# Optimization experiments

Hardware: AMD Instinct MI355X
Metric: run time of the kernel (lower is better)

Reference implementation:

```python
import jax, jax.numpy as jnp
import numpy as np

# dims
B, L, DIN = 32, 1024, 8
D, KK, S = 128, 16, 8
K = (L - KK) // S + 1  # 127 patch tokens
NB, F = 4, 24
Q = 256.0  # Q8.8 scale


def _ste(x, y):
    # straight-through: forward = y (quantized), backward = identity
    return x + jax.lax.stop_gradient(y - x)


def q88(x):
    q = jnp.clip(jnp.round(x * Q), -32768.0, 32767.0) / Q
    return _ste(x, q)


def sig_lut(x):
    xq = q88(x)
    return q88(jax.nn.sigmoid(xq))


def silu_lut(x):
    xq = q88(x)
    return q88(xq * jax.nn.sigmoid(xq))


def layernorm(x, g, b, eps=1e-5):
    m = jnp.mean(x, axis=-1, keepdims=True)
    v = jnp.mean((x - m) ** 2, axis=-1, keepdims=True)
    return (x - m) * jax.lax.rsqrt(v + eps) * g + b


def conv1x1_q88(x, w, b):
    # x: (B, Cin, L); w: (Cout, Cin); Q8.8 integer-emulated pointwise conv
    y = jnp.einsum('bcl,oc->bol', q88(x), q88(w)) + q88(b)[None, :, None]
    return q88(y)


def conv1d_q88(x, w, b, stride):
    # x: (B, Cin, L); w: (Cout, Cin, k)
    y = jax.lax.conv_general_dilated(q88(x), q88(w), (stride,), 'VALID',
                                     dimension_numbers=('NCH', 'OIH', 'NCH'))
    return q88(y + q88(b)[None, :, None])


def ssm_scan(x, w_dt, b_dt):
    # x: (B, K, D). dt_proj acts along the time axis (Linear K->K), per source.
    # lam_all[b,t,d] = sigmoid_LUT(sum_k x[b,k,d] * w_dt[t,k] + b_dt[t])
    lam = sig_lut(jnp.einsum('bkd,tk->btd', x, w_dt) + b_dt[None, :, None])
    xs = jnp.moveaxis(x, 1, 0)      # (K, B, D)
    lams = jnp.moveaxis(lam, 1, 0)  # (K, B, D)

    def step(s, tu):
        lam_t, u_t = tu
        s = lam_t * s + (1.0 - lam_t) * u_t
        return s, s

    s0 = jnp.zeros(x.shape[::2], dtype=x.dtype)  # (B, D)
    _, ys = jax.lax.scan(step, s0, (lams, xs))
    return jnp.moveaxis(ys, 0, 1)  # (B, K, D)


def setup_inputs() -> dict:
    key = jax.random.key(0)
    ks = jax.random.split(key, 20)
    n = lambda k, sh, s=0.05: (jax.random.normal(k, sh, dtype=jnp.float32) * s)
    return {
        'x': jax.random.normal(ks[0], (B, L, DIN), dtype=jnp.float32),
        'w_proj': n(ks[1], (D, DIN), 0.2), 'b_proj': n(ks[2], (D,), 0.02),
        'w_patch': n(ks[3], (D, D, KK), 0.05), 'b_patch': n(ks[4], (D,), 0.02),
        'pe': n(ks[5], (K, D), 0.5), 'pe_scale': jnp.float32(1.0),
        'ln_g': jnp.ones((NB, D), jnp.float32), 'ln_b': jnp.zeros((NB, D), jnp.float32),
        'w_in': n(ks[6], (NB, D, D), 0.08), 'w_gate': n(ks[7], (NB, D, D), 0.08),
        'w_out': n(ks[8], (NB, D, D), 0.08),
        'w_dt': n(ks[9], (NB, K, K), 0.08), 'b_dt': n(ks[10], (NB, K), 0.02),
        'lnf_g': jnp.ones((D,), jnp.float32), 'lnf_b': jnp.zeros((D,), jnp.float32),
        'w_flat': n(ks[11], (D * F, D, K), 0.02), 'b_flat': n(ks[12], (D * F,), 0.02),
        'w_head': n(ks[13], (2, D), 0.1), 'b_head': n(ks[14], (2,), 0.02),
    }


def reference(x, w_proj, b_proj, w_patch, b_patch, pe, pe_scale,
              ln_g, ln_b, w_in, w_gate, w_out, w_dt, b_dt,
              lnf_g, lnf_b, w_flat, b_flat, w_head, b_head):
    xc = jnp.transpose(x, (0, 2, 1))                # (B, DIN, L)
    xp = conv1x1_q88(xc, w_proj, b_proj)            # (B, D, L)
    xe = conv1d_q88(xp, w_patch, b_patch, S)        # (B, D, K)
    h = jnp.transpose(xe, (0, 2, 1)) + pe_scale * pe[None]  # (B, K, D)
    for i in range(NB):
        hn = layernorm(h, ln_g[i], ln_b[i])
        u = silu_lut(jnp.einsum('bkd,de->bke', hn, w_in[i]))
        y = ssm_scan(u, w_dt[i], b_dt[i])
        g = silu_lut(jnp.einsum('bkd,de->bke', hn, w_gate[i]))
        h = h + jnp.einsum('bkd,de->bke', y * g, w_out[i])
    h = layernorm(h, lnf_g, lnf_b)
    xp2 = jnp.transpose(h, (0, 2, 1))               # (B, D, K)
    # output_layer_flat: full-length Conv1d kernel==K -> one giant contraction
    y_feat = q88(jnp.einsum('bdk,odk->bo', q88(xp2), q88(w_flat)) + q88(b_flat))
    y_feat = y_feat.reshape(x.shape[0], D, F)       # (B, D, F)
    out = conv1x1_q88(y_feat, w_head, b_head)       # (B, 2, F)
    return out
```

## Files before the change

kernel.cpp:

```cpp
#include <hip/hip_runtime.h>
#include <cmath>

#define DEV __device__ __forceinline__

namespace {

constexpr int Kp    = 127;
constexpr int Mrows = 32 * Kp;
constexpr int Rred  = 128 * Kp;

DEV float q88(float x) {
  float r = rintf(x * 256.0f);
  r = fminf(fmaxf(r, -32768.0f), 32767.0f);
  return r * 0.00390625f;
}
DEV float sigmoid_(float x) { return 1.0f / (1.0f + expf(-x)); }

DEV void fma16(const float4 av, const float4 bv, float (&acc)[4][4]) {
  acc[0][0] = fmaf(av.x, bv.x, acc[0][0]); acc[0][1] = fmaf(av.x, bv.y, acc[0][1]);
  acc[0][2] = fmaf(av.x, bv.z, acc[0][2]); acc[0][3] = fmaf(av.x, bv.w, acc[0][3]);
  acc[1][0] = fmaf(av.y, bv.x, acc[1][0]); acc[1][1] = fmaf(av.y, bv.y, acc[1][1]);
  acc[1][2] = fmaf(av.y, bv.z, acc[1][2]); acc[1][3] = fmaf(av.y, bv.w, acc[1][3]);
  acc[2][0] = fmaf(av.z, bv.x, acc[2][0]); acc[2][1] = fmaf(av.z, bv.y, acc[2][1]);
  acc[2][2] = fmaf(av.z, bv.z, acc[2][2]); acc[2][3] = fmaf(av.z, bv.w, acc[2][3]);
  acc[3][0] = fmaf(av.w, bv.x, acc[3][0]); acc[3][1] = fmaf(av.w, bv.y, acc[3][1]);
  acc[3][2] = fmaf(av.w, bv.z, acc[3][2]); acc[3][3] = fmaf(av.w, bv.w, acc[3][3]);
}

__global__ __launch_bounds__(256) void k_quant(
    const float* __restrict__ wproj, const float* __restrict__ bproj,
    const float* __restrict__ wpatch, const float* __restrict__ bpatch,
    const float* __restrict__ whead, const float* __restrict__ bhead,
    const float* __restrict__ bflat,
    float* __restrict__ wq_proj, float* __restrict__ bq_proj, float* __restrict__ wpq,
    float* __restrict__ bq_patch, float* __restrict__ wq_head, float* __restrict__ bq_head,
    float* __restrict__ bq_flat) {
  int i = blockIdx.x * 256 + threadIdx.x;
  if (i < 262144) {
    int j = i >> 14;
    int c = (i >> 7) & 127;
    int d = i & 127;
    wpq[i] = q88(wpatch[(d * 128 + c) * 16 + j]);
  }
  int t = i - 262144;
  if (t >= 0) {
    if      (t < 1024) wq_proj[t]         = q88(wproj[t]);
    else if (t < 1152) bq_proj[t - 1024]  = q88(bproj[t - 1024]);
    else if (t < 1280) bq_patch[t - 1152] = q88(bpatch[t - 1152]);
    else if (t < 1536) wq_head[t - 1280]  = q88(whead[t - 1280]);
    else if (t < 1538) bq_head[t - 1536]  = q88(bhead[t - 1536]);
    else if (t < 4610) bq_flat[t - 1538]  = q88(bflat[t - 1538]);
  }
}

__global__ __launch_bounds__(256) void k_proj(const float* __restrict__ x, const float* __restrict__ wq,
                                              const float* __restrict__ bq, float* __restrict__ xpq) {
  int bl0 = blockIdx.x * 16;
  int tid = threadIdx.x;
  __shared__ float xs[128];
  if (tid < 128) xs[tid] = q88(x[(size_t)bl0 * 8 + tid]);
  __syncthreads();
  int o = tid & 127;
  int half = tid >> 7;
  float wv[8];
#pragma unroll
  for (int c = 0; c < 8; ++c) wv[c] = wq[o * 8 + c];
  float bb = bq[o];
#pragma unroll
  for (int il = 0; il < 8; ++il) {
    int l_loc = half * 8 + il;
    float acc = bb;
#pragma unroll
    for (int c = 0; c < 8; ++c) acc = fmaf(xs[l_loc * 8 + c], wv[c], acc);
    xpq[(size_t)(bl0 + l_loc) * 128 + o] = q88(acc);
  }
}

__global__ __launch_bounds__(256) void k_patch(const float* __restrict__ xpq, const float* __restrict__ wpq,
                                               float* __restrict__ partJ) {
  __shared__ __align__(16) float As[128][36];
  int mt = blockIdx.x, jg = blockIdx.y;
  int tid = threadIdx.x;
  int mr = tid & 31, c0 = (tid >> 5) * 16;
  int tn = tid & 31, tm8 = tid >> 5;
  int m0 = mt * 32;
  int g = m0 + mr;
  int bb = g / 127, kq = g % 127;
  float acc[4][4] = {};
  for (int jj = 0; jj < 4; ++jj) {
    int j = jg * 4 + jj;
    const float* src = xpq + ((size_t)bb * 1024 + kq * 8 + j) * 128 + c0;
    __syncthreads();
#pragma unroll
    for (int q = 0; q < 4; ++q) {
      float4 v = *reinterpret_cast<const float4*>(src + q * 4);
      As[c0 + q * 4 + 0][mr] = v.x;
      As[c0 + q * 4 + 1][mr] = v.y;
      As[c0 + q * 4 + 2][mr] = v.z;
      As[c0 + q * 4 + 3][mr] = v.w;
    }
    __syncthreads();
    const float* wp = wpq + (size_t)j * 16384 + tn * 4;
#pragma unroll 4
    for (int c = 0; c < 128; ++c) {
      float4 bv = *reinterpret_cast<const float4*>(wp + c * 128);
      float4 av = *reinterpret_cast<const float4*>(&As[c][tm8 * 4]);
      fma16(av, bv, acc);
    }
  }
  float* dst = partJ + ((size_t)jg * Mrows + m0) * 128 + tn * 4;
#pragma unroll
  for (int i = 0; i < 4; ++i) {
    float4 o4 = make_float4(acc[i][0], acc[i][1], acc[i][2], acc[i][3]);
    *reinterpret_cast<float4*>(dst + (size_t)(tm8 * 4 + i) * 128) = o4;
  }
}

__global__ __launch_bounds__(256) void k_combine(const float* __restrict__ partJ, const float* __restrict__ bqp,
                                                 const float* __restrict__ pe, const float* __restrict__ pesc,
                                                 float* __restrict__ h) {
  int i = blockIdx.x * 256 + threadIdx.x;
  int n = i & 127;
  int gq = i >> 7;
  int k = gq % 127;
  float s = partJ[i] + partJ[520192 + i] + partJ[2 * 520192 + i] + partJ[3 * 520192 + i] + bqp[n];
  h[i] = q88(s) + pesc[0] * pe[k * 128 + n];
}

__global__ __launch_bounds__(256) void k_ln_ug2(const float* __restrict__ h, const float* __restrict__ lng,
                                                const float* __restrict__ lnb, const float* __restrict__ Win,
                                                const float* __restrict__ Wgate, float* __restrict__ u,
                                                float* __restrict__ gbuf) {
  __shared__ __align__(16) float As[128][36];
  __shared__ float2 lnpart[8][32];
  __shared__ float mean_s[32], inv_s[32];
  int tid = threadIdx.x;
  int mr = tid & 31, c0 = (tid >> 5) * 16;
  int m0 = blockIdx.x * 32;
  const float* src = h + (size_t)(m0 + mr) * 128 + c0;
  float s1 = 0.f, s2 = 0.f;
#pragma unroll
  for (int q = 0; q < 4; ++q) {
    float4 v = *reinterpret_cast<const float4*>(src + q * 4);
    As[c0 + q * 4 + 0][mr] = v.x;
    As[c0 + q * 4 + 1][mr] = v.y;
    As[c0 + q * 4 + 2][mr] = v.z;
    As[c0 + q * 4 + 3][mr] = v.w;
    s1 += v.x + v.y + v.z + v.w;
    s2 = fmaf(v.x, v.x, s2); s2 = fmaf(v.y, v.y, s2);
    s2 = fmaf(v.z, v.z, s2); s2 = fmaf(v.w, v.w, s2);
  }
  lnpart[tid >> 5][mr] = make_float2(s1, s2);
  __syncthreads();
  if (tid < 32) {
    float s = 0.f, ss = 0.f;
#pragma unroll
    for (int j = 0; j < 8; ++j) { float2 p = lnpart[j][tid]; s += p.x; ss += p.y; }
    float mn = s * (1.0f / 128.0f);
    float var = ss * (1.0f / 128.0f) - mn * mn;
    mean_s[tid] = mn;
    inv_s[tid] = rsqrtf(var + 1e-5f);
  }
  __syncthreads();
  float mnv = mean_s[mr], invv = inv_s[mr];
#pragma unroll
  for (int q = 0; q < 16; ++q) {
    int c = c0 + q;
    As[c][mr] = (As[c][mr] - mnv) * invv * lng[c] + lnb[c];
  }
  __syncthreads();
  int tn = tid & 31, tm8 = tid >> 5;
  float accU[4][4] = {}, accG[4][4] = {};
  const float* wpU = Win + tn * 4;
  const float* wpG = Wgate + tn * 4;
#pragma unroll 2
  for (int c = 0; c < 128; ++c) {
    float4 av = *reinterpret_cast<const float4*>(&As[c][tm8 * 4]);
    float4 bu = *reinterpret_cast<const float4*>(wpU + c * 128);
    fma16(av, bu, accU);
    float4 bg = *reinterpret_cast<const float4*>(wpG + c * 128);
    fma16(av, bg, accG);
  }
  float* dstU = u + (size_t)m0 * 128 + tn * 4;
  float* dstG = gbuf + (size_t)m0 * 128 + tn * 4;
#pragma unroll
  for (int i = 0; i < 4; ++i) {
    float4 o4;
    { float xq = q88(accU[i][0]); o4.x = q88(xq * sigmoid_(xq)); }
    { float xq = q88(accU[i][1]); o4.y = q88(xq * sigmoid_(xq)); }
    { float xq = q88(accU[i][2]); o4.z = q88(xq * sigmoid_(xq)); }
    { float xq = q88(accU[i][3]); o4.w = q88(xq * sigmoid_(xq)); }
    *reinterpret_cast<float4*>(dstU + (size_t)(tm8 * 4 + i) * 128) = o4;
    float4 g4;
    { float xq = q88(accG[i][0]); g4.x = q88(xq * sigmoid_(xq)); }
    { float xq = q88(accG[i][1]); g4.y = q88(xq * sigmoid_(xq)); }
    { float xq = q88(accG[i][2]); g4.z = q88(xq * sigmoid_(xq)); }
    { float xq = q88(accG[i][3]); g4.w = q88(xq * sigmoid_(xq)); }
    *reinterpret_cast<float4*>(dstG + (size_t)(tm8 * 4 + i) * 128) = g4;
  }
}

__global__ __launch_bounds__(256) void k_lamg(const float* __restrict__ u, const float* __restrict__ wdt,
                                              const float* __restrict__ bdt, float* __restrict__ lam) {
  __shared__ __align__(16) float Wk[32][36];
  __shared__ __align__(16) float Us[32][132];
  int b = blockIdx.x, tt = blockIdx.y;
  int t0 = tt * 32;
  int tid = threadIdx.x;
  int dg = tid & 31, tg = tid >> 5;
  float acc[4][4] = {};
  const float* ub = u + (size_t)b * (127 * 128);
  for (int k0 = 0; k0 < 127; k0 += 32) {
    __syncthreads();
    {
      int k = tid & 31, tl = tid >> 5;
#pragma unroll
      for (int q = 0; q < 4; ++q) {
        int t = tl + 8 * q;
        int tg2 = t0 + t, kg = k0 + k;
        float v = (tg2 < 127 && kg < 127) ? wdt[tg2 * 127 + kg] : 0.f;
        Wk[k][t] = v;
      }
    }
    {
      int dq = tid & 7, k = tid >> 3;
      int kg = k0 + k;
      const float* srcp = ub + (size_t)kg * 128 + dq * 16;
#pragma unroll
      for (int q = 0; q < 4; ++q) {
        float4 v = make_float4(0.f, 0.f, 0.f, 0.f);
        if (kg < 127) v = *reinterpret_cast<const float4*>(srcp + q * 4);
        *reinterpret_cast<float4*>(&Us[k][dq * 16 + q * 4]) = v;
      }
    }
    __syncthreads();
#pragma unroll 4
    for (int k = 0; k < 32; ++k) {
      float4 tv = *reinterpret_cast<const float4*>(&Wk[k][tg * 4]);
      float4 dv = *reinterpret_cast<const float4*>(&Us[k][dg * 4]);
      fma16(tv, dv, acc);
    }
  }
#pragma unroll
  for (int ti = 0; ti < 4; ++ti) {
    int t = t0 + tg * 4 + ti;
    if (t < 127) {
      float bb = bdt[t];
      float4 o4;
      o4.x = q88(sigmoid_(q88(acc[ti][0] + bb)));
      o4.y = q88(sigmoid_(q88(acc[ti][1] + bb)));
      o4.z = q88(sigmoid_(q88(acc[ti][2] + bb)));
      o4.w = q88(sigmoid_(q88(acc[ti][3] + bb)));
      *reinterpret_cast<float4*>(lam + ((size_t)b * 127 + t) * 128 + dg * 4) = o4;
    }
  }
}

__global__ __launch_bounds__(128) void k_scan(const float* __restrict__ u, const float* __restrict__ gbuf,
                                              float* __restrict__ lamp) {
  int b = blockIdx.x, d = threadIdx.x;
  const size_t base = (size_t)b * (127 * 128) + d;
  float lm[8], uu[8], gg[8];
#pragma unroll
  for (int j = 0; j < 8; ++j) {
    size_t idx = base + (size_t)j * 128;
    lm[j] = lamp[idx]; uu[j] = u[idx]; gg[j] = gbuf[idx];
  }
  float s = 0.f;
  int t = 0;
  for (int it = 0; it < 15; ++it) {
#pragma unroll
    for (int j = 0; j < 8; ++j) {
      float l0 = lm[j], u0 = uu[j], g0 = gg[j];
      s = l0 * s + (1.0f - l0) * u0;
      lamp[base + (size_t)(t + j) * 128] = s * g0;
      int tn = t + j + 8;
      if (tn < 127) {
        size_t idx = base + (size_t)tn * 128;
        lm[j] = lamp[idx]; uu[j] = u[idx]; gg[j] = gbuf[idx];
      }
    }
    t += 8;
  }
#pragma unroll
  for (int j = 0; j < 7; ++j) {
    float l0 = lm[j], u0 = uu[j], g0 = gg[j];
    s = l0 * s + (1.0f - l0) * u0;
    lamp[base + (size_t)(120 + j) * 128] = s * g0;
  }
}

__global__ __launch_bounds__(256) void k_outproj(const float* __restrict__ p, const float* __restrict__ W,
                                                 float* __restrict__ h) {
  __shared__ __align__(16) float As[128][36];
  int tid = threadIdx.x;
  int mr = tid & 31, c0 = (tid >> 5) * 16;
  int m0 = blockIdx.x * 32;
  const float* src = p + (size_t)(m0 + mr) * 128 + c0;
#pragma unroll
  for (int q = 0; q < 4; ++q) {
    float4 v = *reinterpret_cast<const float4*>(src + q * 4);
    As[c0 + q * 4 + 0][mr] = v.x;
    As[c0 + q * 4 + 1][mr] = v.y;
    As[c0 + q * 4 + 2][mr] = v.z;
    As[c0 + q * 4 + 3][mr] = v.w;
  }
  __syncthreads();
  int tn = tid & 31, tm8 = tid >> 5;
  float acc[4][4] = {};
  const float* wp = W + tn * 4;
#pragma unroll 4
  for (int c = 0; c < 128; ++c) {
    float4 bv = *reinterpret_cast<const float4*>(wp + c * 128);
    float4 av = *reinterpret_cast<const float4*>(&As[c][tm8 * 4]);
    fma16(av, bv, acc);
  }
  float* dst = h + (size_t)m0 * 128 + tn * 4;
#pragma unroll
  for (int i = 0; i < 4; ++i) {
    float4 hv = *reinterpret_cast<float4*>(dst + (size_t)(tm8 * 4 + i) * 128);
    hv.x += acc[i][0]; hv.y += acc[i][1]; hv.z += acc[i][2]; hv.w += acc[i][3];
    *reinterpret_cast<float4*>(dst + (size_t)(tm8 * 4 + i) * 128) = hv;
  }
}

__global__ __launch_bounds__(128) void k_lnf(const float* __restrict__ h, const float* __restrict__ gg,
                                             const float* __restrict__ bb, float* __restrict__ xp2q) {
  int row = blockIdx.x;
  int d = threadIdx.x;
  float v = h[(size_t)row * 128 + d];
  float a = v, sq = v * v;
#pragma unroll
  for (int off = 32; off >= 1; off >>= 1) {
    a += __shfl_xor(a, off, 64);
    sq += __shfl_xor(sq, off, 64);
  }
  __shared__ float ps[2][2];
  int w = d >> 6;
  if ((d & 63) == 0) { ps[w][0] = a; ps[w][1] = sq; }
  __syncthreads();
  float S1 = ps[0][0] + ps[1][0], S2 = ps[0][1] + ps[1][1];
  float mn = S1 * (1.0f / 128.0f);
  float inv = rsqrtf(S2 * (1.0f / 128.0f) - mn * mn + 1e-5f);
  float hn = (v - mn) * inv * gg[d] + bb[d];
  int b = row / 127, k = row % 127;
  xp2q[((size_t)b * 128 + d) * 127 + k] = q88(hn);
}

__global__ __launch_bounds__(128) void k_flat(const float* __restrict__ Aq, const float* __restrict__ Wf,
                                              float* __restrict__ partF) {
  __shared__ float As[32][36];
  __shared__ float Ws[32][132];
  int ot = blockIdx.x, rs = blockIdx.y;
  int tid = threadIdx.x;
  int og = tid & 31, bsub = tid >> 5;
  int o0 = ot * 128;
  int r0 = rs * 256;
  float acc[8][4] = {};

  const int wq4 = tid & 3;
  const int wrow_l = tid >> 2;
  const int aq = tid >> 5;
  const int ab = tid & 31;

  float4 wreg[4][2];
  float4 areg[2];

  auto loadch = [&](int rb) {
#pragma unroll
    for (int p = 0; p < 4; ++p) {
      const float* wrow = Wf + (size_t)(o0 + wrow_l + 32 * p) * Rred;
#pragma unroll
      for (int q = 0; q < 2; ++q) {
        int rr = rb + wq4 * 8 + q * 4;
        wreg[p][q] = (rr < Rred) ? *reinterpret_cast<const float4*>(wrow + rr)
                                 : make_float4(0.f, 0.f, 0.f, 0.f);
      }
    }
#pragma unroll
    for (int i = 0; i < 2; ++i) {
      int rr = rb + aq * 4 + 16 * i;
      areg[i] = (rr < Rred) ? *reinterpret_cast<const float4*>(Aq + (size_t)ab * Rred + rr)
                            : make_float4(0.f, 0.f, 0.f, 0.f);
    }
  };

  loadch(r0);
  for (int ch = 0; ch < 8; ++ch) {
    __syncthreads();
#pragma unroll
    for (int p = 0; p < 4; ++p) {
      int oc = wrow_l + 32 * p;
#pragma unroll
      for (int q = 0; q < 2; ++q) {
        int rl = wq4 * 8 + q * 4;
        Ws[rl + 0][oc] = rintf(wreg[p][q].x * 256.0f);
        Ws[rl + 1][oc] = rintf(wreg[p][q].y * 256.0f);
        Ws[rl + 2][oc] = rintf(wreg[p][q].z * 256.0f);
        Ws[rl + 3][oc] = rintf(wreg[p][q].w * 256.0f);
      }
    }
#pragma unroll
    for (int i = 0; i < 2; ++i) {
      int rl = aq * 4 + 16 * i;
      As[rl + 0][ab] = areg[i].x * 0.00390625f;
      As[rl + 1][ab] = areg[i].y * 0.00390625f;
      As[rl + 2][ab] = areg[i].z * 0.00390625f;
      As[rl + 3][ab] = areg[i].w * 0.00390625f;
    }
    __syncthreads();
    if (ch < 7) loadch(r0 + (ch + 1) * 32);
#pragma unroll 4
    for (int rl = 0; rl < 32; ++rl) {
      float4 w  = *reinterpret_cast<const float4*>(&Ws[rl][og * 4]);
      float4 a0 = *reinterpret_cast<const float4*>(&As[rl][bsub * 8]);
      float4 a1 = *reinterpret_cast<const float4*>(&As[rl][bsub * 8 + 4]);
      float a[8] = {a0.x, a0.y, a0.z, a0.w, a1.x, a1.y, a1.z, a1.w};
#pragma unroll
      for (int bi = 0; bi < 8; ++bi) {
        acc[bi][0] = fmaf(a[bi], w.x, acc[bi][0]);
        acc[bi][1] = fmaf(a[bi], w.y, acc[bi][1]);
        acc[bi][2] = fmaf(a[bi], w.z, acc[bi][2]);
        acc[bi][3] = fmaf(a[bi], w.w, acc[bi][3]);
      }
    }
  }
#pragma unroll
  for (int bi = 0; bi < 8; ++bi) {
    int b = bsub * 8 + bi;
    float* dst = partF + ((size_t)rs * 32 + b) * 3072 + o0 + og * 4;
    *reinterpret_cast<float4*>(dst) = make_float4(acc[bi][0], acc[bi][1], acc[bi][2], acc[bi][3]);
  }
}

__global__ __launch_bounds__(256) void k_head(const float* __restrict__ partF, const float* __restrict__ bqf,
                                              const float* __restrict__ wqh, const float* __restrict__ bqh,
                                              float* __restrict__ out) {
  int b = blockIdx.x;
  int tid = threadIdx.x;
  __shared__ float yf[3072];
#pragma unroll
  for (int i = 0; i < 12; ++i) {
    int o = tid + 256 * i;
    float s = bqf[o];
    for (int rsq = 0; rsq < 64; ++rsq) s += partF[((size_t)rsq * 32 + b) * 3072 + o];
    yf[o] = q88(s);
  }
  __syncthreads();
  if (tid < 48) {
    int oh = tid / 24, f = tid % 24;
    float acc = bqh[oh];
    for (int d = 0; d < 128; ++d) acc = fmaf(yf[d * 24 + f], wqh[oh * 128 + d], acc);
    out[(size_t)b * 48 + oh * 24 + f] = q88(acc);
  }
}

}

extern "C" void kernel_launch(void* const* d_in, const int* in_sizes, int n_in,
                              void* d_out, int out_size, void* d_ws, size_t ws_size,
                              hipStream_t stream) {
  const float* x      = (const float*)d_in[0];
  const float* wproj  = (const float*)d_in[1];
  const float* bproj  = (const float*)d_in[2];
  const float* wpatch = (const float*)d_in[3];
  const float* bpatch = (const float*)d_in[4];
  const float* pe     = (const float*)d_in[5];
  const float* pescal = (const float*)d_in[6];
  const float* lng    = (const float*)d_in[7];
  const float* lnb    = (const float*)d_in[8];
  const float* win    = (const float*)d_in[9];
  const float* wgate  = (const float*)d_in[10];
  const float* wout   = (const float*)d_in[11];
  const float* wdt    = (const float*)d_in[12];
  const float* bdt    = (const float*)d_in[13];
  const float* lnfg   = (const float*)d_in[14];
  const float* lnfb   = (const float*)d_in[15];
  const float* wflat  = (const float*)d_in[16];
  const float* bflat  = (const float*)d_in[17];
  const float* whead  = (const float*)d_in[18];
  const float* bhead  = (const float*)d_in[19];
  float* out = (float*)d_out;
  float* ws  = (float*)d_ws;

  constexpr size_t O_WQPROJ  = 0;
  constexpr size_t O_BQPROJ  = 1024;
  constexpr size_t O_WPQ     = 2048;
  constexpr size_t O_BQPATCH = 264192;
  constexpr size_t O_WQHEAD  = 264320;
  constexpr size_t O_BQHEAD  = 264576;
  constexpr size_t O_BQFLAT  = 264704;
  constexpr size_t O_XPQ     = 267776;
  constexpr size_t O_PARTJ   = 4462080;
  constexpr size_t O_H       = 6542848;
  constexpr size_t O_U       = 7063040;
  constexpr size_t O_G       = 7583232;
  constexpr size_t O_LAMP    = 8103424;
  constexpr size_t O_XP2Q    = 8623616;
  constexpr size_t O_PARTF   = O_XPQ;

  k_quant<<<(262144 + 4610 + 255) / 256, 256, 0, stream>>>(
      wproj, bproj, wpatch, bpatch, whead, bhead, bflat,
      ws + O_WQPROJ, ws + O_BQPROJ, ws + O_WPQ, ws + O_BQPATCH,
      ws + O_WQHEAD, ws + O_BQHEAD, ws + O_BQFLAT);

  k_proj<<<2048, 256, 0, stream>>>(x, ws + O_WQPROJ, ws + O_BQPROJ, ws + O_XPQ);

  {
    dim3 g(127, 4);
    k_patch<<<g, 256, 0, stream>>>(ws + O_XPQ, ws + O_WPQ, ws + O_PARTJ);
  }
  k_combine<<<2032, 256, 0, stream>>>(ws + O_PARTJ, ws + O_BQPATCH, pe, pescal, ws + O_H);

  for (int i = 0; i < 4; ++i) {
    k_ln_ug2<<<127, 256, 0, stream>>>(ws + O_H, lng + i * 128, lnb + i * 128,
                                      win + (size_t)i * 16384, wgate + (size_t)i * 16384,
                                      ws + O_U, ws + O_G);
    {
      dim3 gl(32, 4);
      k_lamg<<<gl, 256, 0, stream>>>(ws + O_U, wdt + (size_t)i * 16129, bdt + (size_t)i * 127,
                                     ws + O_LAMP);
    }
    k_scan<<<32, 128, 0, stream>>>(ws + O_U, ws + O_G, ws + O_LAMP);
    k_outproj<<<127, 256, 0, stream>>>(ws + O_LAMP, wout + (size_t)i * 16384, ws + O_H);
  }

  k_lnf<<<4064, 128, 0, stream>>>(ws + O_H, lnfg, lnfb, ws + O_XP2Q);

  {
    dim3 g(24, 64);
    k_flat<<<g, 128, 0, stream>>>(ws + O_XP2Q, wflat, ws + O_PARTF);
  }
  k_head<<<32, 256, 0, stream>>>(ws + O_PARTF, ws + O_BQFLAT, ws + O_WQHEAD, ws + O_BQHEAD, out);
}
```

Before: 445.3 us.

## Fuse dt-projection with scan, and out-proj with next block's LN and projections

Merges the lambda projection and sequential scan into one kernel per (batch, 32-channel slice), keeping u, gate and lambda tiles in shared memory so lambda is never written out and read back. Fuses the output projection and residual add with the next block's layernorm and in/gate projections, and the last one with the final layernorm. This cuts the launches per block from four to two and removes intermediate global traffic. In exchange the scan now runs on only 32 threads per block and the lambda GEMM is recomputed over the full K in each block, reloading W_dt per tile.

```diff
diff --git a/kernel.cpp b/kernel.cpp
--- a/kernel.cpp
+++ b/kernel.cpp
@@ -200,151 +200,285 @@
   }
 }
 
-__global__ __launch_bounds__(256) void k_lamg(const float* __restrict__ u, const float* __restrict__ wdt,
-                                              const float* __restrict__ bdt, float* __restrict__ lam) {
-  __shared__ __align__(16) float Wk[32][36];
-  __shared__ __align__(16) float Us[32][132];
-  int b = blockIdx.x, tt = blockIdx.y;
-  int t0 = tt * 32;
-  int tid = threadIdx.x;
-  int dg = tid & 31, tg = tid >> 5;
-  float acc[4][4] = {};
-  const float* ub = u + (size_t)b * (127 * 128);
-  for (int k0 = 0; k0 < 127; k0 += 32) {
-    __syncthreads();
-    {
-      int k = tid & 31, tl = tid >> 5;
-#pragma unroll
-      for (int q = 0; q < 4; ++q) {
-        int t = tl + 8 * q;
-        int tg2 = t0 + t, kg = k0 + k;
-        float v = (tg2 < 127 && kg < 127) ? wdt[tg2 * 127 + kg] : 0.f;
-        Wk[k][t] = v;
+__global__ __launch_bounds__(256) void k_lam_scan(const float* __restrict__ u, const float* __restrict__ gbuf,
+                                                  const float* __restrict__ wdt, const float* __restrict__ bdt,
+                                                  float* __restrict__ p) {
+  __shared__ float Us[127][33];
+  __shared__ float Gs[127][33];
+  __shared__ float Wt[32][128];
+  __shared__ float Lt[32][33];
+  __shared__ float Pt[32][33];
+  int b = blockIdx.x, d0 = blockIdx.y * 32;
+  int tid = threadIdx.x;
+  {
+    int d = tid & 31;
+    int kb = tid >> 5;
+#pragma unroll
+    for (int pass = 0; pass < 16; ++pass) {
+      int k = kb + pass * 8;
+      if (k < 127) {
+        size_t idx = ((size_t)b * 127 + k) * 128 + d0 + d;
+        Us[k][d] = u[idx];
+        Gs[k][d] = gbuf[idx];
       }
     }
-    {
-      int dq = tid & 7, k = tid >> 3;
-      int kg = k0 + k;
-      const float* srcp = ub + (size_t)kg * 128 + dq * 16;
-#pragma unroll
-      for (int q = 0; q < 4; ++q) {
-        float4 v = make_float4(0.f, 0.f, 0.f, 0.f);
-        if (kg < 127) v = *reinterpret_cast<const float4*>(srcp + q * 4);
-        *reinterpret_cast<float4*>(&Us[k][dq * 16 + q * 4]) = v;
+  }
+  __syncthreads();
+  int dg = tid & 31, t4 = tid >> 5;
+  float s = 0.f;
+  for (int tt = 0; tt < 4; ++tt) {
+    int t0 = tt * 32;
+    int tn_tile = (t0 + 32 <= 127) ? 32 : (127 - t0);
+#pragma unroll
+    for (int pass = 0; pass < 16; ++pass) {
+      int e = pass * 256 + tid;
+      int t = e >> 7, k = e & 127;
+      float v = 0.f;
+      if (k < 127 && t < tn_tile) v = wdt[(t0 + t) * 127 + k];
+      Wt[t][k] = v;
+    }
+    __syncthreads();
+    float a0 = 0.f, a1 = 0.f, a2 = 0.f, a3 = 0.f;
+    const int tb = t4 * 4;
+#pragma unroll 4
+    for (int k = 0; k < 127; ++k) {
+      float a = Us[k][dg];
+      a0 = fmaf(a, Wt[tb + 0][k], a0);
+      a1 = fmaf(a, Wt[tb + 1][k], a1);
+      a2 = fmaf(a, Wt[tb + 2][k], a2);
+      a3 = fmaf(a, Wt[tb + 3][k], a3);
+    }
+    if (tb + 0 < tn_tile) Lt[tb + 0][dg] = q88(sigmoid_(q88(a0 + bdt[t0 + tb + 0])));
+    if (tb + 1 < tn_tile) Lt[tb + 1][dg] = q88(sigmoid_(q88(a1 + bdt[t0 + tb + 1])));
+    if (tb + 2 < tn_tile) Lt[tb + 2][dg] = q88(sigmoid_(q88(a2 + bdt[t0 + tb + 2])));
+    if (tb + 3 < tn_tile) Lt[tb + 3][dg] = q88(sigmoid_(q88(a3 + bdt[t0 + tb + 3])));
+    __syncthreads();
+    if (tid < 32) {
+      int d = tid;
+      for (int j = 0; j < tn_tile; ++j) {
+        float lm = Lt[j][d];
+        float uu = Us[t0 + j][d];
+        s = lm * s + (1.0f - lm) * uu;
+        Pt[j][d] = s * Gs[t0 + j][d];
       }
     }
     __syncthreads();
-#pragma unroll 4
-    for (int k = 0; k < 32; ++k) {
-      float4 tv = *reinterpret_cast<const float4*>(&Wk[k][tg * 4]);
-      float4 dv = *reinterpret_cast<const float4*>(&Us[k][dg * 4]);
-      fma16(tv, dv, acc);
-    }
-  }
-#pragma unroll
-  for (int ti = 0; ti < 4; ++ti) {
-    int t = t0 + tg * 4 + ti;
-    if (t < 127) {
-      float bb = bdt[t];
-      float4 o4;
-      o4.x = q88(sigmoid_(q88(acc[ti][0] + bb)));
-      o4.y = q88(sigmoid_(q88(acc[ti][1] + bb)));
-      o4.z = q88(sigmoid_(q88(acc[ti][2] + bb)));
-      o4.w = q88(sigmoid_(q88(acc[ti][3] + bb)));
-      *reinterpret_cast<float4*>(lam + ((size_t)b * 127 + t) * 128 + dg * 4) = o4;
-    }
-  }
-}
-
-__global__ __launch_bounds__(128) void k_scan(const float* __restrict__ u, const float* __restrict__ gbuf,
-                                              float* __restrict__ lamp) {
-  int b = blockIdx.x, d = threadIdx.x;
-  const size_t base = (size_t)b * (127 * 128) + d;
-  float lm[8], uu[8], gg[8];
-#pragma unroll
-  for (int j = 0; j < 8; ++j) {
-    size_t idx = base + (size_t)j * 128;
-    lm[j] = lamp[idx]; uu[j] = u[idx]; gg[j] = gbuf[idx];
-  }
-  float s = 0.f;
-  int t = 0;
-  for (int it = 0; it < 15; ++it) {
-#pragma unroll
-    for (int j = 0; j < 8; ++j) {
-      float l0 = lm[j], u0 = uu[j], g0 = gg[j];
-      s = l0 * s + (1.0f - l0) * u0;
-      lamp[base + (size_t)(t + j) * 128] = s * g0;
-      int tn = t + j + 8;
-      if (tn < 127) {
-        size_t idx = base + (size_t)tn * 128;
-        lm[j] = lamp[idx]; uu[j] = u[idx]; gg[j] = gbuf[idx];
-      }
-    }
-    t += 8;
-  }
-#pragma unroll
-  for (int j = 0; j < 7; ++j) {
-    float l0 = lm[j], u0 = uu[j], g0 = gg[j];
-    s = l0 * s + (1.0f - l0) * u0;
-    lamp[base + (size_t)(120 + j) * 128] = s * g0;
-  }
-}
-
-__global__ __launch_bounds__(256) void k_outproj(const float* __restrict__ p, const float* __restrict__ W,
-                                                 float* __restrict__ h) {
+#pragma unroll
+    for (int pass = 0; pass < 4; ++pass) {
+      int e = pass * 256 + tid;
+      int t = e >> 5, d = e & 31;
+      if (t < tn_tile)
+        p[((size_t)b * 127 + t0 + t) * 128 + d0 + d] = Pt[t][d];
+    }
+    __syncthreads();
+  }
+}
+
+__global__ __launch_bounds__(256) void k_out_ln_ug(
+    const float* __restrict__ p, const float* __restrict__ Wout, float* __restrict__ h,
+    const float* __restrict__ lng, const float* __restrict__ lnb,
+    const float* __restrict__ Win, const float* __restrict__ Wgate,
+    float* __restrict__ u, float* __restrict__ gbuf) {
   __shared__ __align__(16) float As[128][36];
+  __shared__ float2 lnpart[8][32];
+  __shared__ float mean_s[32], inv_s[32];
   int tid = threadIdx.x;
   int mr = tid & 31, c0 = (tid >> 5) * 16;
   int m0 = blockIdx.x * 32;
-  const float* src = p + (size_t)(m0 + mr) * 128 + c0;
-#pragma unroll
-  for (int q = 0; q < 4; ++q) {
-    float4 v = *reinterpret_cast<const float4*>(src + q * 4);
-    As[c0 + q * 4 + 0][mr] = v.x;
-    As[c0 + q * 4 + 1][mr] = v.y;
-    As[c0 + q * 4 + 2][mr] = v.z;
-    As[c0 + q * 4 + 3][mr] = v.w;
+  {
+    const float* src = p + (size_t)(m0 + mr) * 128 + c0;
+#pragma unroll
+    for (int q = 0; q < 4; ++q) {
+      float4 v = *reinterpret_cast<const float4*>(src + q * 4);
+      As[c0 + q * 4 + 0][mr] = v.x;
+      As[c0 + q * 4 + 1][mr] = v.y;
+      As[c0 + q * 4 + 2][mr] = v.z;
+      As[c0 + q * 4 + 3][mr] = v.w;
+    }
   }
   __syncthreads();
   int tn = tid & 31, tm8 = tid >> 5;
   float acc[4][4] = {};
-  const float* wp = W + tn * 4;
+  {
+    const float* wp = Wout + tn * 4;
 #pragma unroll 4
+    for (int c = 0; c < 128; ++c) {
+      float4 bv = *reinterpret_cast<const float4*>(wp + c * 128);
+      float4 av = *reinterpret_cast<const float4*>(&As[c][tm8 * 4]);
+      fma16(av, bv, acc);
+    }
+  }
+  float4 hv[4];
+  {
+    float* hdst = h + (size_t)m0 * 128 + tn * 4;
+#pragma unroll
+    for (int i = 0; i < 4; ++i) {
+      hv[i] = *reinterpret_cast<float4*>(hdst + (size_t)(tm8 * 4 + i) * 128);
+      hv[i].x += acc[i][0]; hv[i].y += acc[i][1]; hv[i].z += acc[i][2]; hv[i].w += acc[i][3];
+      *reinterpret_cast<float4*>(hdst + (size_t)(tm8 * 4 + i) * 128) = hv[i];
+    }
+  }
+  __syncthreads();
+#pragma unroll
+  for (int i = 0; i < 4; ++i) {
+    int row = tm8 * 4 + i;
+    As[tn * 4 + 0][row] = hv[i].x;
+    As[tn * 4 + 1][row] = hv[i].y;
+    As[tn * 4 + 2][row] = hv[i].z;
+    As[tn * 4 + 3][row] = hv[i].w;
+  }
+  __syncthreads();
+  {
+    float s1 = 0.f, s2 = 0.f;
+#pragma unroll
+    for (int q = 0; q < 4; ++q) {
+      float vx = As[c0 + q * 4 + 0][mr];
+      float vy = As[c0 + q * 4 + 1][mr];
+      float vz = As[c0 + q * 4 + 2][mr];
+      float vw = As[c0 + q * 4 + 3][mr];
+      s1 += vx + vy + vz + vw;
+      s2 = fmaf(vx, vx, s2); s2 = fmaf(vy, vy, s2);
+      s2 = fmaf(vz, vz, s2); s2 = fmaf(vw, vw, s2);
+    }
+    lnpart[tid >> 5][mr] = make_float2(s1, s2);
+  }
+  __syncthreads();
+  if (tid < 32) {
+    float s = 0.f, ss = 0.f;
+#pragma unroll
+    for (int j = 0; j < 8; ++j) { float2 pp = lnpart[j][tid]; s += pp.x; ss += pp.y; }
+    float mn = s * (1.0f / 128.0f);
+    float var = ss * (1.0f / 128.0f) - mn * mn;
+    mean_s[tid] = mn;
+    inv_s[tid] = rsqrtf(var + 1e-5f);
+  }
+  __syncthreads();
+  {
+    float mnv = mean_s[mr], invv = inv_s[mr];
+#pragma unroll
+    for (int q = 0; q < 16; ++q) {
+      int c = c0 + q;
+      As[c][mr] = (As[c][mr] - mnv) * invv * lng[c] + lnb[c];
+    }
+  }
+  __syncthreads();
+  float accU[4][4] = {}, accG[4][4] = {};
+  const float* wpU = Win + tn * 4;
+  const float* wpG = Wgate + tn * 4;
+#pragma unroll 2
   for (int c = 0; c < 128; ++c) {
-    float4 bv = *reinterpret_cast<const float4*>(wp + c * 128);
     float4 av = *reinterpret_cast<const float4*>(&As[c][tm8 * 4]);
-    fma16(av, bv, acc);
-  }
-  float* dst = h + (size_t)m0 * 128 + tn * 4;
+    float4 bu = *reinterpret_cast<const float4*>(wpU + c * 128);
+    fma16(av, bu, accU);
+    float4 bg = *reinterpret_cast<const float4*>(wpG + c * 128);
+    fma16(av, bg, accG);
+  }
+  float* dstU = u + (size_t)m0 * 128 + tn * 4;
+  float* dstG = gbuf + (size_t)m0 * 128 + tn * 4;
 #pragma unroll
   for (int i = 0; i < 4; ++i) {
-    float4 hv = *reinterpret_cast<float4*>(dst + (size_t)(tm8 * 4 + i) * 128);
-    hv.x += acc[i][0]; hv.y += acc[i][1]; hv.z += acc[i][2]; hv.w += acc[i][3];
-    *reinterpret_cast<float4*>(dst + (size_t)(tm8 * 4 + i) * 128) = hv;
-  }
-}
-
-__global__ __launch_bounds__(128) void k_lnf(const float* __restrict__ h, const float* __restrict__ gg,
-                                             const float* __restrict__ bb, float* __restrict__ xp2q) {
-  int row = blockIdx.x;
-  int d = threadIdx.x;
-  float v = h[(size_t)row * 128 + d];
-  float a = v, sq = v * v;
-#pragma unroll
-  for (int off = 32; off >= 1; off >>= 1) {
-    a += __shfl_xor(a, off, 64);
-    sq += __shfl_xor(sq, off, 64);
-  }
-  __shared__ float ps[2][2];
-  int w = d >> 6;
-  if ((d & 63) == 0) { ps[w][0] = a; ps[w][1] = sq; }
-  __syncthreads();
-  float S1 = ps[0][0] + ps[1][0], S2 = ps[0][1] + ps[1][1];
-  float mn = S1 * (1.0f / 128.0f);
-  float inv = rsqrtf(S2 * (1.0f / 128.0f) - mn * mn + 1e-5f);
-  float hn = (v - mn) * inv * gg[d] + bb[d];
-  int b = row / 127, k = row % 127;
-  xp2q[((size_t)b * 128 + d) * 127 + k] = q88(hn);
+    float4 o4;
+    { float xq = q88(accU[i][0]); o4.x = q88(xq * sigmoid_(xq)); }
+    { float xq = q88(accU[i][1]); o4.y = q88(xq * sigmoid_(xq)); }
+    { float xq = q88(accU[i][2]); o4.z = q88(xq * sigmoid_(xq)); }
+    { float xq = q88(accU[i][3]); o4.w = q88(xq * sigmoid_(xq)); }
+    *reinterpret_cast<float4*>(dstU + (size_t)(tm8 * 4 + i) * 128) = o4;
+    float4 g4;
+    { float xq = q88(accG[i][0]); g4.x = q88(xq * sigmoid_(xq)); }
+    { float xq = q88(accG[i][1]); g4.y = q88(xq * sigmoid_(xq)); }
+    { float xq = q88(accG[i][2]); g4.z = q88(xq * sigmoid_(xq)); }
+    { float xq = q88(accG[i][3]); g4.w = q88(xq * sigmoid_(xq)); }
+    *reinterpret_cast<float4*>(dstG + (size_t)(tm8 * 4 + i) * 128) = g4;
+  }
+}
+
+__global__ __launch_bounds__(256) void k_out_lnf(
+    const float* __restrict__ p, const float* __restrict__ Wout, const float* __restrict__ h,
+    const float* __restrict__ gg, const float* __restrict__ bb, float* __restrict__ xp2q) {
+  __shared__ __align__(16) float As[128][36];
+  __shared__ float2 lnpart[8][32];
+  __shared__ float mean_s[32], inv_s[32];
+  int tid = threadIdx.x;
+  int mr = tid & 31, c0 = (tid >> 5) * 16;
+  int m0 = blockIdx.x * 32;
+  {
+    const float* src = p + (size_t)(m0 + mr) * 128 + c0;
+#pragma unroll
+    for (int q = 0; q < 4; ++q) {
+      float4 v = *reinterpret_cast<const float4*>(src + q * 4);
+      As[c0 + q * 4 + 0][mr] = v.x;
+      As[c0 + q * 4 + 1][mr] = v.y;
+      As[c0 + q * 4 + 2][mr] = v.z;
+      As[c0 + q * 4 + 3][mr] = v.w;
+    }
+  }
+  __syncthreads();
+  int tn = tid & 31, tm8 = tid >> 5;
+  float acc[4][4] = {};
+  {
+    const float* wp = Wout + tn * 4;
+#pragma unroll 4
+    for (int c = 0; c < 128; ++c) {
+      float4 bv = *reinterpret_cast<const float4*>(wp + c * 128);
+      float4 av = *reinterpret_cast<const float4*>(&As[c][tm8 * 4]);
+      fma16(av, bv, acc);
+    }
+  }
+  float4 hv[4];
+  {
+    const float* hsrc = h + (size_t)m0 * 128 + tn * 4;
+#pragma unroll
+    for (int i = 0; i < 4; ++i) {
+      hv[i] = *reinterpret_cast<const float4*>(hsrc + (size_t)(tm8 * 4 + i) * 128);
+      hv[i].x += acc[i][0]; hv[i].y += acc[i][1]; hv[i].z += acc[i][2]; hv[i].w += acc[i][3];
+    }
+  }
+  __syncthreads();
+#pragma unroll
+  for (int i = 0; i < 4; ++i) {
+    int row = tm8 * 4 + i;
+    As[tn * 4 + 0][row] = hv[i].x;
+    As[tn * 4 + 1][row] = hv[i].y;
+    As[tn * 4 + 2][row] = hv[i].z;
+    As[tn * 4 + 3][row] = hv[i].w;
+  }
+  __syncthreads();
+  {
+    float s1 = 0.f, s2 = 0.f;
+#pragma unroll
+    for (int q = 0; q < 4; ++q) {
+      float vx = As[c0 + q * 4 + 0][mr];
+      float vy = As[c0 + q * 4 + 1][mr];
+      float vz = As[c0 + q * 4 + 2][mr];
+      float vw = As[c0 + q * 4 + 3][mr];
+      s1 += vx + vy + vz + vw;
+      s2 = fmaf(vx, vx, s2); s2 = fmaf(vy, vy, s2);
+      s2 = fmaf(vz, vz, s2); s2 = fmaf(vw, vw, s2);
+    }
+    lnpart[tid >> 5][mr] = make_float2(s1, s2);
+  }
+  __syncthreads();
+  if (tid < 32) {
+    float s = 0.f, ss = 0.f;
+#pragma unroll
+    for (int j = 0; j < 8; ++j) { float2 pp = lnpart[j][tid]; s += pp.x; ss += pp.y; }
+    float mn = s * (1.0f / 128.0f);
+    float var = ss * (1.0f / 128.0f) - mn * mn;
+    mean_s[tid] = mn;
+    inv_s[tid] = rsqrtf(var + 1e-5f);
+  }
+  __syncthreads();
+  {
+    float mnv = mean_s[mr], invv = inv_s[mr];
+    int row = m0 + mr;
+    int b = row / 127, k = row % 127;
+#pragma unroll
+    for (int q = 0; q < 16; ++q) {
+      int c = c0 + q;
+      float hn = (As[c][mr] - mnv) * invv * gg[c] + bb[c];
+      xp2q[((size_t)b * 128 + c) * 127 + k] = q88(hn);
+    }
+  }
 }
 
 __global__ __launch_bounds__(128) void k_flat(const float* __restrict__ Aq, const float* __restrict__ Wf,
@@ -495,7 +629,7 @@
   constexpr size_t O_H       = 6542848;
   constexpr size_t O_U       = 7063040;
   constexpr size_t O_G       = 7583232;
-  constexpr size_t O_LAMP    = 8103424;
+  constexpr size_t O_P       = 8103424;
   constexpr size_t O_XP2Q    = 8623616;
   constexpr size_t O_PARTF   = O_XPQ;
 
@@ -512,20 +646,23 @@
   }
   k_combine<<<2032, 256, 0, stream>>>(ws + O_PARTJ, ws + O_BQPATCH, pe, pescal, ws + O_H);
 
+  k_ln_ug2<<<127, 256, 0, stream>>>(ws + O_H, lng, lnb, win, wgate, ws + O_U, ws + O_G);
+
   for (int i = 0; i < 4; ++i) {
-    k_ln_ug2<<<127, 256, 0, stream>>>(ws + O_H, lng + i * 128, lnb + i * 128,
-                                      win + (size_t)i * 16384, wgate + (size_t)i * 16384,
-                                      ws + O_U, ws + O_G);
-    {
-      dim3 gl(32, 4);
-      k_lamg<<<gl, 256, 0, stream>>>(ws + O_U, wdt + (size_t)i * 16129, bdt + (size_t)i * 127,
-                                     ws + O_LAMP);
-    }
-    k_scan<<<32, 128, 0, stream>>>(ws + O_U, ws + O_G, ws + O_LAMP);
-    k_outproj<<<127, 256, 0, stream>>>(ws + O_LAMP, wout + (size_t)i * 16384, ws + O_H);
-  }
-
-  k_lnf<<<4064, 128, 0, stream>>>(ws + O_H, lnfg, lnfb, ws + O_XP2Q);
+    dim3 gl(32, 4);
+    k_lam_scan<<<gl, 256, 0, stream>>>(ws + O_U, ws + O_G, wdt + (size_t)i * 16129,
+                                       bdt + (size_t)i * 127, ws + O_P);
+    if (i < 3) {
+      k_out_ln_ug<<<127, 256, 0, stream>>>(ws + O_P, wout + (size_t)i * 16384, ws + O_H,
+                                           lng + (i + 1) * 128, lnb + (i + 1) * 128,
+                                           win + (size_t)(i + 1) * 16384,
+                                           wgate + (size_t)(i + 1) * 16384,
+                                           ws + O_U, ws + O_G);
+    } else {
+      k_out_lnf<<<127, 256, 0, stream>>>(ws + O_P, wout + (size_t)i * 16384, ws + O_H,
+                                         lnfg, lnfb, ws + O_XP2Q);
+    }
+  }
 
   {
     dim3 g(24, 64);
```

After: 520.6 us. 16.9% more time.
